# Optimization experiments

Hardware: AMD Instinct MI355X
Metric: run time of the kernel (lower is better)

The kernel has to match this reference:

```python
import jax, jax.numpy as jnp
import numpy as np

N_HEADS = 12
MAX_POS = 2048
SEQ = MAX_POS - 2  # seq_len_without_special = 2046
HEAD_DIM = 64
BATCH = 8


def setup_inputs() -> dict:
    key = jax.random.key(0)
    k1, k2, k3 = jax.random.split(key, 3)
    v = jax.random.normal(k1, (BATCH, MAX_POS, N_HEADS, HEAD_DIM), jnp.float32)
    offset = jax.random.normal(k2, (1, N_HEADS), jnp.float32)
    # learned bias base, torch init: uniform(-0.1, 0.1), shape [1, H, SEQ] (symmetric)
    w = jax.random.uniform(k3, (1, N_HEADS, SEQ), jnp.float32, -0.1, 0.1)
    return {"v": v, "offset": offset, "w": w}


def _fft_bias(v, offset, w):
    # strip special tokens ([CLS]/[SEP])
    v_ = v[:, 1:-1, :, :]                      # [B, S, H, D]
    B, S, H, D = v_.shape
    # --- symmetric circulant base z of length 2S-1 ---
    w_ = w[..., :S]                            # [1, H, S]
    z = jnp.concatenate(
        [w_[..., -1:], jnp.flip(w_[..., 1:], axis=-1), w_[..., :-1]], axis=-1
    )                                          # [1, H, 2S-1]
    z = z - offset[..., None]                  # broadcast offset per head
    z = jnp.exp(z)                             # feature_map == 'exp'
    z_fft = jnp.fft.rfft(z)                    # [1, H, S] complex (len 2S-1 odd -> m=S)

    pad = S - 1                                # symmetric: pad_size = seq_len - 1
    v_p = jnp.transpose(v_, (0, 3, 2, 1))      # [B, D, H, S]
    v_p = jnp.pad(v_p, ((0, 0), (0, 0), (0, 0), (pad, 0)))  # left-pad to 2S-1
    v_fft = jnp.fft.rfft(v_p)                  # [B, D, H, S]
    # torch.irfft(x, 1) with default signal_sizes infers even length 2*(m-1)=2S-2
    pbv = jnp.fft.irfft(v_fft * z_fft)[..., :S]  # [B, D, H, S]
    pbv = jnp.pad(pbv, ((0, 0), (0, 0), (0, 0), (1, 1)))     # restore special slots
    pbv = jnp.transpose(pbv, (0, 3, 2, 1))     # [B, S+2, H, D]

    o = jnp.pad(jnp.ones((S,), v.dtype), (pad, 0))           # [2S-1]
    o_fft = jnp.fft.rfft(o)                    # [S]
    z_pb = jnp.fft.irfft(z_fft * o_fft)[..., :S]             # [1, H, S]
    z_pb = jnp.pad(z_pb, ((0, 0), (0, 0), (1, 1)))           # [1, H, S+2]
    z_pb = jnp.swapaxes(z_pb, -2, -1)          # [1, S+2, H]
    return pbv, z_pb


def reference(v, offset, w):
    return _fft_bias(v, offset, w)
```

## Files before the change

kernel.cpp:

```cpp
#include <hip/hip_runtime.h>
#include <hip/hip_bf16.h>

#define BATCH 8
#define MAXPOS 2048
#define SEQ 2046
#define NH 12
#define HD 64
#define NCSLOT 254
#define TSTEPS 64
#define PLANE (NH * HD)

typedef __attribute__((ext_vector_type(4))) float floatx4;
typedef __attribute__((ext_vector_type(8))) short shortx8;

#define ATILE_BYTES (NH * NCSLOT * 512 * 2)

#define GLOAD_LDS16(src, dst)                                                  \
    __builtin_amdgcn_global_load_lds(                                          \
        (const __attribute__((address_space(1))) void*)(src),                  \
        (__attribute__((address_space(3))) void*)(dst), 16, 0, 0)

#define NB_V   (TSTEPS * NH * BATCH)
#define NB_ZPB NH
#define NB_A   (NCSLOT * NH)

__global__ __launch_bounds__(256)
void prep_all(const float* __restrict__ v, const float* __restrict__ w,
              const float* __restrict__ off, ushort* __restrict__ atile,
              ushort* __restrict__ vbf, float* __restrict__ out) {
    const int bi  = blockIdx.x;
    const int tid = threadIdx.x;

    if (bi < NB_V) {
        __shared__ float Ls[32][64];
        const int tc = bi & 63;
        int rem = bi >> 6;
        const int h = rem % NH;
        const int b = rem / NH;
#pragma unroll
        for (int i = 0; i < 2; ++i) {
            int idx = tid + 256 * i;
            int row = idx >> 4;
            int c4  = (idx & 15) * 4;
            int key = (row >> 3) * 16;
            int t   = tc * 32 + row;
            float4 val = make_float4(0.f, 0.f, 0.f, 0.f);
            if (t < SEQ) val = *(const float4*)(v + ((size_t)(b * MAXPOS + 1 + t) * NH + h) * HD + c4);
            *(float4*)&Ls[row][c4 ^ key] = val;
        }
        __syncthreads();
        const int wv   = tid >> 6;
        const int lane = tid & 63;
        const int q    = lane >> 4;
        const int dcol = lane & 15;
        ushort pk[8];
#pragma unroll
        for (int j = 0; j < 8; ++j) {
            __hip_bfloat16 bv = __float2bfloat16(Ls[q * 8 + j][(wv * 16 + dcol) ^ (q * 16)]);
            pk[j] = *(ushort*)&bv;
        }
        *(uint4*)(vbf + ((size_t)((b * NH + h) * TSTEPS + tc) * 4 + wv) * 512 + lane * 8) = *(uint4*)pk;
    } else if (bi < NB_V + NB_ZPB) {
        __shared__ float Es[SEQ];
        __shared__ float Ss[SEQ];
        __shared__ float wsum[4];
        const int h    = bi - NB_V;
        const int wid  = tid >> 6;
        const int lane = tid & 63;
        const float offh = off[h];
        const float* wh  = w + h * SEQ;
        for (int i = tid; i < SEQ; i += 256) Es[i] = __expf(wh[i] - offh);
        __syncthreads();
        const int base = tid * 8;
        float loc[8];
        float s = 0.f;
#pragma unroll
        for (int j = 0; j < 8; ++j) {
            float e = (base + j < SEQ) ? Es[base + j] : 0.f;
            s += e; loc[j] = s;
        }
        float sc = s;
#pragma unroll
        for (int d = 1; d < 64; d <<= 1) {
            float t = __shfl_up(sc, d);
            if (lane >= d) sc += t;
        }
        if (lane == 63) wsum[wid] = sc;
        __syncthreads();
        float woff = 0.f;
        for (int k = 0; k < wid; ++k) woff += wsum[k];
        float prefix = woff + sc - s;
#pragma unroll
        for (int j = 0; j < 8; ++j)
            if (base + j < SEQ) Ss[base + j] = prefix + loc[j];
        __syncthreads();
        const float E0 = Es[0];
        const size_t zb = (size_t)BATCH * MAXPOS * PLANE;
        for (int i = tid; i < SEQ; i += 256)
            out[zb + (size_t)(i + 1) * NH + h] = Ss[i] + Ss[SEQ - 1 - i] - E0;
    } else if (bi < NB_V + NB_ZPB + NB_A) {
        const int idx   = bi - NB_V - NB_ZPB;
        const int cslot = idx % NCSLOT;
        const int h     = idx / NCSLOT;
        const float offh = off[h];
        const float* wh  = w + h * SEQ;
        const int ci   = cslot - 127;
        const int lane = tid >> 2;
        const int jp   = (tid & 3) * 2;
        const int q    = lane >> 4;
        const int m    = lane & 15;
        const int d0   = 16 * ci + q * 8 - m + jp;
        ushort pk[2];
#pragma unroll
        for (int e = 0; e < 2; ++e) {
            int k = d0 + e; k = (k < 0) ? -k : k;
            float val = (k < SEQ) ? __expf(wh[k] - offh) : 0.f;
            __hip_bfloat16 bv = __float2bfloat16(val);
            pk[e] = *(ushort*)&bv;
        }
        *(ushort2*)(atile + ((size_t)(h * NCSLOT + cslot) * 512 + lane * 8 + jp)) = *(ushort2*)pk;
    } else {
        const int i = (bi - NB_V - NB_ZPB - NB_A) * 256 + tid;
        if (i < 2 * BATCH * PLANE) {
            int side = i / (BATCH * PLANE);
            int r    = i % (BATCH * PLANE);
            int b    = r / PLANE;
            int j    = r % PLANE;
            int p    = side ? (MAXPOS - 1) : 0;
            out[((size_t)b * MAXPOS + p) * PLANE + j] = 0.f;
        }
        if (i < 2 * NH) {
            size_t zb = (size_t)BATCH * MAXPOS * PLANE;
            int p = (i < NH) ? 0 : (MAXPOS - 1);
            out[zb + (size_t)p * NH + (i % NH)] = 0.f;
        }
    }
}


#define FENCE    asm volatile("" ::: "memory")
#define WAITBAR6 asm volatile("s_waitcnt vmcnt(6)\n\ts_barrier" ::: "memory")
#define WAITBAR0 asm volatile("s_waitcnt vmcnt(0)\n\ts_barrier" ::: "memory")

#define GEMM_STEP(CK, NXT, BS, STG)                                            \
  do {                                                                         \
    shortx8 aa[4];                                                             \
    _Pragma("unroll")                                                          \
    for (int s = 0; s < 4; ++s)                                                \
        aa[s] = *(const shortx8*)(aRb + (CK) * 4096 + s * 512);                \
    if (STG) {                                                                 \
        GLOAD_LDS16(aQ + (CK) * 1024,       aWb + (NXT) * 4096);               \
        GLOAD_LDS16(aQ + (CK) * 1024 - 512, aWb + (NXT) * 4096 + 512);         \
    }                                                                          \
    __builtin_amdgcn_s_setprio(1);                                             \
    _Pragma("unroll")                                                          \
    for (int s = 0; s < 4; ++s)                                                \
        _Pragma("unroll")                                                      \
        for (int dt = 0; dt < 4; ++dt)                                         \
            acc[s][dt] = __builtin_amdgcn_mfma_f32_16x16x32_bf16(              \
                aa[s], b[BS][dt], acc[s][dt], 0, 0, 0);                        \
    __builtin_amdgcn_s_setprio(0);                                             \
    if (STG) {                                                                 \
        _Pragma("unroll")                                                      \
        for (int dt = 0; dt < 4; ++dt)                                         \
            b[BS][dt] = *(const shortx8*)(bQ + (CK) * 2048 + dt * 512);        \
    }                                                                          \
  } while (0)

__global__ __launch_bounds__(256, 3)
void gemm_pbv(const ushort* __restrict__ atile, const ushort* __restrict__ vbf,
              float* __restrict__ out) {
    __shared__ short As[4][8 * 512];

    const int bid  = blockIdx.x;
    const int slot = bid >> 3;
    const int g    = (bid & 7) * 6 + (slot % 6);
    const int nt   = slot / 6;
    const int h    = g >> 2;
    const int bq   = g & 3;
    const int tid  = threadIdx.x;
    const int wv   = tid >> 6;
    const int lane = tid & 63;
    const int sh   = wv >> 1;
    const int bw   = wv & 1;
    const int bb   = bq * 2 + bw;

    floatx4 acc[4][4];
#pragma unroll
    for (int s = 0; s < 4; ++s)
#pragma unroll
        for (int dt = 0; dt < 4; ++dt) acc[s][dt] = (floatx4){0.f, 0.f, 0.f, 0.f};

    const ushort* aS = atile + ((size_t)h * NCSLOT + (127 - nt * 8 - 2 * wv)) * 512 + lane * 8;
    const ushort* bP = vbf + (size_t)(bb * NH + h) * (TSTEPS * 4 * 512) + lane * 8;
    short* aWb = &As[0][2 * wv * 512];
    const short* aRb = &As[0][sh * 4 * 512] + lane * 8;

    shortx8 b[2][4];

    GLOAD_LDS16(aS,       aWb);
    GLOAD_LDS16(aS - 512, aWb + 512);
#pragma unroll
    for (int dt = 0; dt < 4; ++dt) b[0][dt] = *(const shortx8*)(bP + dt * 512);
    FENCE;
    GLOAD_LDS16(aS + 1024, aWb + 4096);
    GLOAD_LDS16(aS + 512,  aWb + 4096 + 512);
#pragma unroll
    for (int dt = 0; dt < 4; ++dt) b[1][dt] = *(const shortx8*)(bP + 2048 + dt * 512);
    WAITBAR6;

    const ushort* aQ = aS + 2 * 1024;
    const ushort* bQ = bP + 2 * 2048;

    for (int u = 0; u < 15; ++u) {
        GEMM_STEP(0, 2, 0, 1); WAITBAR6;
        GEMM_STEP(1, 3, 1, 1); WAITBAR6;
        GEMM_STEP(2, 0, 0, 1); WAITBAR6;
        GEMM_STEP(3, 1, 1, 1); WAITBAR6;
        aQ += 4 * 1024;
        bQ += 4 * 2048;
    }
    GEMM_STEP(0, 2, 0, 1); WAITBAR6;
    GEMM_STEP(1, 3, 1, 1); WAITBAR6;
    GEMM_STEP(2, 0, 0, 0); WAITBAR0;
    GEMM_STEP(3, 1, 1, 0);

    const int q    = lane >> 4;
    const int dcol = lane & 15;
    const int nB   = nt * 128 + sh * 64;
#pragma unroll
    for (int s = 0; s < 4; ++s) {
        int nsb = nB + s * 16 + q * 4;
#pragma unroll
        for (int r = 0; r < 4; ++r) {
            int n = nsb + r;
            if (n < SEQ) {
                float* ob = out + ((size_t)(bb * MAXPOS + 1 + n) * NH + h) * HD + dcol;
#pragma unroll
                for (int dt = 0; dt < 4; ++dt) ob[dt * 16] = acc[s][dt][r];
            }
        }
    }
}

extern "C" void kernel_launch(void* const* d_in, const int* in_sizes, int n_in,
                              void* d_out, int out_size, void* d_ws, size_t ws_size,
                              hipStream_t stream) {
    const float* v   = (const float*)d_in[0];
    const float* off = (const float*)d_in[1];
    const float* w   = (const float*)d_in[2];
    float* out = (float*)d_out;

    ushort* atile = (ushort*)d_ws;
    ushort* vbf   = (ushort*)((char*)d_ws + ATILE_BYTES);

    prep_all<<<NB_V + NB_ZPB + NB_A + 48, 256, 0, stream>>>(v, w, off, atile, vbf, out);
    gemm_pbv<<<768, 256, 0, stream>>>(atile, vbf, out);
}
```

Measured before the change: 144.3 us.

## Give each wave a private LDS ring to drop block-wide barriers in GEMM

```diff
diff --git a/kernel.cpp b/kernel.cpp
--- a/kernel.cpp
+++ b/kernel.cpp
@@ -138,19 +138,21 @@
 }
 
 
-#define FENCE    asm volatile("" ::: "memory")
-#define WAITBAR6 asm volatile("s_waitcnt vmcnt(6)\n\ts_barrier" ::: "memory")
-#define WAITBAR0 asm volatile("s_waitcnt vmcnt(0)\n\ts_barrier" ::: "memory")
-
-#define GEMM_STEP(CK, NXT, BS, STG)                                            \
+#define FENCE  asm volatile("" ::: "memory")
+#define WAITV8 asm volatile("s_waitcnt vmcnt(8)" ::: "memory")
+#define WAITV0 asm volatile("s_waitcnt vmcnt(0)" ::: "memory")
+
+#define GEMM_STEP(RING, NXT, BS, STG, E)                                       \
   do {                                                                         \
     shortx8 aa[4];                                                             \
     _Pragma("unroll")                                                          \
     for (int s = 0; s < 4; ++s)                                                \
-        aa[s] = *(const shortx8*)(aRb + (CK) * 4096 + s * 512);                \
+        aa[s] = *(const shortx8*)(aR + (RING) * 2048 + s * 512);               \
     if (STG) {                                                                 \
-        GLOAD_LDS16(aQ + (CK) * 1024,       aWb + (NXT) * 4096);               \
-        GLOAD_LDS16(aQ + (CK) * 1024 - 512, aWb + (NXT) * 4096 + 512);         \
+        GLOAD_LDS16(aQ + (2 * (E) - 0) * 512, aW + (NXT) * 2048 + 0 * 512);    \
+        GLOAD_LDS16(aQ + (2 * (E) - 1) * 512, aW + (NXT) * 2048 + 1 * 512);    \
+        GLOAD_LDS16(aQ + (2 * (E) - 2) * 512, aW + (NXT) * 2048 + 2 * 512);    \
+        GLOAD_LDS16(aQ + (2 * (E) - 3) * 512, aW + (NXT) * 2048 + 3 * 512);    \
     }                                                                          \
     __builtin_amdgcn_s_setprio(1);                                             \
     _Pragma("unroll")                                                          \
@@ -163,27 +165,24 @@
     if (STG) {                                                                 \
         _Pragma("unroll")                                                      \
         for (int dt = 0; dt < 4; ++dt)                                         \
-            b[BS][dt] = *(const shortx8*)(bQ + (CK) * 2048 + dt * 512);        \
+            b[BS][dt] = *(const shortx8*)(bQ + (E) * 2048 + dt * 512);         \
     }                                                                          \
   } while (0)
 
 __global__ __launch_bounds__(256, 3)
 void gemm_pbv(const ushort* __restrict__ atile, const ushort* __restrict__ vbf,
               float* __restrict__ out) {
-    __shared__ short As[4][8 * 512];
-
-    const int bid  = blockIdx.x;
-    const int slot = bid >> 3;
-    const int g    = (bid & 7) * 6 + (slot % 6);
-    const int nt   = slot / 6;
-    const int h    = g >> 2;
-    const int bq   = g & 3;
-    const int tid  = threadIdx.x;
-    const int wv   = tid >> 6;
-    const int lane = tid & 63;
-    const int sh   = wv >> 1;
-    const int bw   = wv & 1;
-    const int bb   = bq * 2 + bw;
+    __shared__ short As[4][3][4][512];
+
+    const int bid     = blockIdx.x;
+    const int logical = (bid & 7) * 96 + (bid >> 3);
+    const int g       = logical >> 3;
+    const int nt      = logical & 7;
+    const int h       = g >> 3;
+    const int bb      = g & 7;
+    const int tid     = threadIdx.x;
+    const int wv      = tid >> 6;
+    const int lane    = tid & 63;
 
     floatx4 acc[4][4];
 #pragma unroll
@@ -191,43 +190,49 @@
 #pragma unroll
         for (int dt = 0; dt < 4; ++dt) acc[s][dt] = (floatx4){0.f, 0.f, 0.f, 0.f};
 
-    const ushort* aS = atile + ((size_t)h * NCSLOT + (127 - nt * 8 - 2 * wv)) * 512 + lane * 8;
+    const ushort* aS = atile + ((size_t)h * NCSLOT + (127 - nt * 16 - wv * 4)) * 512 + lane * 8;
     const ushort* bP = vbf + (size_t)(bb * NH + h) * (TSTEPS * 4 * 512) + lane * 8;
-    short* aWb = &As[0][2 * wv * 512];
-    const short* aRb = &As[0][sh * 4 * 512] + lane * 8;
+    short*       aW = &As[wv][0][0][0];
+    const short* aR = &As[wv][0][0][0] + lane * 8;
 
     shortx8 b[2][4];
 
-    GLOAD_LDS16(aS,       aWb);
-    GLOAD_LDS16(aS - 512, aWb + 512);
+    GLOAD_LDS16(aS - 0 * 512, aW + 0 * 512);
+    GLOAD_LDS16(aS - 1 * 512, aW + 1 * 512);
+    GLOAD_LDS16(aS - 2 * 512, aW + 2 * 512);
+    GLOAD_LDS16(aS - 3 * 512, aW + 3 * 512);
 #pragma unroll
     for (int dt = 0; dt < 4; ++dt) b[0][dt] = *(const shortx8*)(bP + dt * 512);
     FENCE;
-    GLOAD_LDS16(aS + 1024, aWb + 4096);
-    GLOAD_LDS16(aS + 512,  aWb + 4096 + 512);
+    GLOAD_LDS16(aS + (2 - 0) * 512, aW + 2048 + 0 * 512);
+    GLOAD_LDS16(aS + (2 - 1) * 512, aW + 2048 + 1 * 512);
+    GLOAD_LDS16(aS + (2 - 2) * 512, aW + 2048 + 2 * 512);
+    GLOAD_LDS16(aS + (2 - 3) * 512, aW + 2048 + 3 * 512);
 #pragma unroll
     for (int dt = 0; dt < 4; ++dt) b[1][dt] = *(const shortx8*)(bP + 2048 + dt * 512);
-    WAITBAR6;
-
-    const ushort* aQ = aS + 2 * 1024;
+    WAITV8;
+
+    const ushort* aQ = aS + 4 * 512;
     const ushort* bQ = bP + 2 * 2048;
 
-    for (int u = 0; u < 15; ++u) {
-        GEMM_STEP(0, 2, 0, 1); WAITBAR6;
-        GEMM_STEP(1, 3, 1, 1); WAITBAR6;
-        GEMM_STEP(2, 0, 0, 1); WAITBAR6;
-        GEMM_STEP(3, 1, 1, 1); WAITBAR6;
-        aQ += 4 * 1024;
-        bQ += 4 * 2048;
+    for (int u = 0; u < 10; ++u) {
+        GEMM_STEP(0, 2, 0, 1, 0); WAITV8;
+        GEMM_STEP(1, 0, 1, 1, 1); WAITV8;
+        GEMM_STEP(2, 1, 0, 1, 2); WAITV8;
+        GEMM_STEP(0, 2, 1, 1, 3); WAITV8;
+        GEMM_STEP(1, 0, 0, 1, 4); WAITV8;
+        GEMM_STEP(2, 1, 1, 1, 5); WAITV8;
+        aQ += 12 * 512;
+        bQ += 6 * 2048;
     }
-    GEMM_STEP(0, 2, 0, 1); WAITBAR6;
-    GEMM_STEP(1, 3, 1, 1); WAITBAR6;
-    GEMM_STEP(2, 0, 0, 0); WAITBAR0;
-    GEMM_STEP(3, 1, 1, 0);
+    GEMM_STEP(0, 2, 0, 1, 0); WAITV8;
+    GEMM_STEP(1, 0, 1, 1, 1); WAITV8;
+    GEMM_STEP(2, 0, 0, 0, 0); WAITV0;
+    GEMM_STEP(0, 0, 1, 0, 0);
 
     const int q    = lane >> 4;
     const int dcol = lane & 15;
-    const int nB   = nt * 128 + sh * 64;
+    const int nB   = nt * 256 + wv * 64;
 #pragma unroll
     for (int s = 0; s < 4; ++s) {
         int nsb = nB + s * 16 + q * 4;
```

New measurement: 151.4 us. 1.05x slower.

## Restructure pbv GEMM tiling with LDS-staged B panel and ring-buffered A

Applied to the files above, without the earlier changes.

```diff
diff --git a/kernel.cpp b/kernel.cpp
--- a/kernel.cpp
+++ b/kernel.cpp
@@ -138,19 +138,27 @@
 }
 
 
-#define FENCE    asm volatile("" ::: "memory")
-#define WAITBAR6 asm volatile("s_waitcnt vmcnt(6)\n\ts_barrier" ::: "memory")
-#define WAITBAR0 asm volatile("s_waitcnt vmcnt(0)\n\ts_barrier" ::: "memory")
-
-#define GEMM_STEP(CK, NXT, BS, STG)                                            \
+#define WBAR                                                                   \
   do {                                                                         \
-    shortx8 aa[4];                                                             \
+    if (wvu < 2) asm volatile("s_waitcnt vmcnt(2)\n\ts_barrier" ::: "memory"); \
+    else         asm volatile("s_waitcnt vmcnt(1)\n\ts_barrier" ::: "memory"); \
+  } while (0)
+#define WBAR0 asm volatile("s_waitcnt vmcnt(0)\n\ts_barrier" ::: "memory")
+
+#define STEP(T4, E, STG)                                                       \
+  do {                                                                         \
+    shortx8 aa[4], bf[4];                                                      \
+    const int abE = ab + 2 * (E);                                              \
     _Pragma("unroll")                                                          \
-    for (int s = 0; s < 4; ++s)                                                \
-        aa[s] = *(const shortx8*)(aRb + (CK) * 4096 + s * 512);                \
+    for (int k = 0; k < 4; ++k)                                                \
+        aa[k] = *(const shortx8*)(&As[(abE - k) & 31][lane8]);                 \
+    _Pragma("unroll")                                                          \
+    for (int dt = 0; dt < 4; ++dt)                                             \
+        bf[dt] = *(const shortx8*)(&Bs[T4][dt][lane8]);                        \
     if (STG) {                                                                 \
-        GLOAD_LDS16(aQ + (CK) * 1024,       aWb + (NXT) * 4096);               \
-        GLOAD_LDS16(aQ + (CK) * 1024 - 512, aWb + (NXT) * 4096 + 512);         \
+        if (wvu < 2)                                                           \
+            GLOAD_LDS16(aSt + (E) * 1024, &As[(csw + 2 * (E)) & 31][0]);       \
+        GLOAD_LDS16(bSt + (E) * 2048, &Bs[((T4) + 2) & 3][wvu][0]);            \
     }                                                                          \
     __builtin_amdgcn_s_setprio(1);                                             \
     _Pragma("unroll")                                                          \
@@ -158,32 +166,27 @@
         _Pragma("unroll")                                                      \
         for (int dt = 0; dt < 4; ++dt)                                         \
             acc[s][dt] = __builtin_amdgcn_mfma_f32_16x16x32_bf16(              \
-                aa[s], b[BS][dt], acc[s][dt], 0, 0, 0);                        \
+                aa[s], bf[dt], acc[s][dt], 0, 0, 0);                           \
     __builtin_amdgcn_s_setprio(0);                                             \
-    if (STG) {                                                                 \
-        _Pragma("unroll")                                                      \
-        for (int dt = 0; dt < 4; ++dt)                                         \
-            b[BS][dt] = *(const shortx8*)(bQ + (CK) * 2048 + dt * 512);        \
-    }                                                                          \
   } while (0)
 
 __global__ __launch_bounds__(256, 3)
 void gemm_pbv(const ushort* __restrict__ atile, const ushort* __restrict__ vbf,
               float* __restrict__ out) {
-    __shared__ short As[4][8 * 512];
+    __shared__ short As[32][512];
+    __shared__ short Bs[4][4][512];
 
     const int bid  = blockIdx.x;
-    const int slot = bid >> 3;
-    const int g    = (bid & 7) * 6 + (slot % 6);
-    const int nt   = slot / 6;
-    const int h    = g >> 2;
-    const int bq   = g & 3;
+    const int l    = (bid & 7) * 96 + (bid >> 3);
+    const int g    = l >> 3;
+    const int nt   = l & 7;
+    const int h    = g >> 3;
+    const int bb   = g & 7;
     const int tid  = threadIdx.x;
-    const int wv   = tid >> 6;
+    const int wvu  = __builtin_amdgcn_readfirstlane(tid >> 6);
     const int lane = tid & 63;
-    const int sh   = wv >> 1;
-    const int bw   = wv & 1;
-    const int bb   = bq * 2 + bw;
+    const int lane8 = lane * 8;
+    const int nt16  = nt * 16;
 
     floatx4 acc[4][4];
 #pragma unroll
@@ -191,43 +194,42 @@
 #pragma unroll
         for (int dt = 0; dt < 4; ++dt) acc[s][dt] = (floatx4){0.f, 0.f, 0.f, 0.f};
 
-    const ushort* aS = atile + ((size_t)h * NCSLOT + (127 - nt * 8 - 2 * wv)) * 512 + lane * 8;
-    const ushort* bP = vbf + (size_t)(bb * NH + h) * (TSTEPS * 4 * 512) + lane * 8;
-    short* aWb = &As[0][2 * wv * 512];
-    const short* aRb = &As[0][sh * 4 * 512] + lane * 8;
-
-    shortx8 b[2][4];
-
-    GLOAD_LDS16(aS,       aWb);
-    GLOAD_LDS16(aS - 512, aWb + 512);
-#pragma unroll
-    for (int dt = 0; dt < 4; ++dt) b[0][dt] = *(const shortx8*)(bP + dt * 512);
-    FENCE;
-    GLOAD_LDS16(aS + 1024, aWb + 4096);
-    GLOAD_LDS16(aS + 512,  aWb + 4096 + 512);
-#pragma unroll
-    for (int dt = 0; dt < 4; ++dt) b[1][dt] = *(const shortx8*)(bP + 2048 + dt * 512);
-    WAITBAR6;
-
-    const ushort* aQ = aS + 2 * 1024;
-    const ushort* bQ = bP + 2 * 2048;
+    const ushort* aBase  = atile + (size_t)h * NCSLOT * 512;
+    const ushort* bPanel = vbf + (size_t)(bb * NH + h) * (TSTEPS * 4 * 512);
+
+    {
+        const int cbase = 112 - nt16;
+        const int j0 = (wvu == 0) ? 0 : (wvu == 1) ? 5 : (wvu == 2) ? 10 : 14;
+        const int j1 = (wvu == 0) ? 5 : (wvu == 1) ? 10 : (wvu == 2) ? 14 : 18;
+        for (int j = j0; j < j1; ++j) {
+            const int cs = cbase + j;
+            GLOAD_LDS16(aBase + (size_t)cs * 512 + lane8, &As[cs & 31][0]);
+        }
+        GLOAD_LDS16(bPanel + (0 * 4 + wvu) * 512 + lane8, &Bs[0][wvu][0]);
+        GLOAD_LDS16(bPanel + (1 * 4 + wvu) * 512 + lane8, &Bs[1][wvu][0]);
+    }
+    WBAR0;
+
+    int ab  = 127 - nt16 - 4 * wvu;
+    int csw = 131 - nt16 - wvu;
+    const ushort* aSt = aBase + (size_t)(131 - nt16 - wvu) * 512 + lane8;
+    const ushort* bSt = bPanel + (2 * 4 + wvu) * 512 + lane8;
 
     for (int u = 0; u < 15; ++u) {
-        GEMM_STEP(0, 2, 0, 1); WAITBAR6;
-        GEMM_STEP(1, 3, 1, 1); WAITBAR6;
-        GEMM_STEP(2, 0, 0, 1); WAITBAR6;
-        GEMM_STEP(3, 1, 1, 1); WAITBAR6;
-        aQ += 4 * 1024;
-        bQ += 4 * 2048;
-    }
-    GEMM_STEP(0, 2, 0, 1); WAITBAR6;
-    GEMM_STEP(1, 3, 1, 1); WAITBAR6;
-    GEMM_STEP(2, 0, 0, 0); WAITBAR0;
-    GEMM_STEP(3, 1, 1, 0);
+        STEP(0, 0, 1); WBAR;
+        STEP(1, 1, 1); WBAR;
+        STEP(2, 2, 1); WBAR;
+        STEP(3, 3, 1); WBAR;
+        ab += 8; csw += 8; aSt += 4 * 1024; bSt += 4 * 2048;
+    }
+    STEP(0, 0, 1); WBAR;
+    STEP(1, 1, 1); WBAR;
+    STEP(2, 2, 0); WBAR0;
+    STEP(3, 3, 0);
 
     const int q    = lane >> 4;
     const int dcol = lane & 15;
-    const int nB   = nt * 128 + sh * 64;
+    const int nB   = nt * 256 + wvu * 64;
 #pragma unroll
     for (int s = 0; s < 4; ++s) {
         int nsb = nB + s * 16 + q * 4;
```

Measured after the change: 137.3 us. 4.9% less time.
